# Optimization experiments

Hardware: AMD Instinct MI355X
Metric: run time of the kernel (lower is better)

Reference implementation:

```python
import jax, jax.numpy as jnp
import numpy as np

B = 2048            # number of session graphs in the batch
ORDER = 3           # multi-order granularities s1, s2, s3
D = 128             # input_dim = hidden_dim = output_dim (fc_out is None)
NODES_PER = (50, 25, 16)   # nodes per graph for s1, s2, s3
NPG = sum(NODES_PER)       # 91 nodes per graph (summed batch_num_nodes)
N = B * NPG                # total flattened nodes


def setup_inputs() -> dict:
    key = jax.random.key(0)
    k0, k1, k2, k3 = jax.random.split(key, 4)
    feats = jax.random.normal(k0, (N, D), dtype=jnp.float32)
    scale = 1.0 / np.sqrt(D).astype(np.float32)
    Wu = jax.random.normal(k1, (ORDER, D, D), dtype=jnp.float32) * scale
    bu = jnp.zeros((ORDER, D), dtype=jnp.float32)
    Wv = jax.random.normal(k2, (ORDER, D, D), dtype=jnp.float32) * scale
    We = jax.random.normal(k3, (ORDER, D), dtype=jnp.float32) * scale
    # segment id per node: idx = cat([ones(batch_num_nodes[j]) * j])
    idx = jnp.repeat(jnp.arange(B, dtype=jnp.int32), NPG)
    # last node of each order's block inside every graph (feats['s_i'][last_nodess[i]])
    offs = np.cumsum([0] + list(NODES_PER))
    last = np.stack([np.arange(B) * NPG + (offs[o + 1] - 1) for o in range(ORDER)])
    last_idx = jnp.asarray(last, dtype=jnp.int32)  # [ORDER, B]
    return {"feats": feats, "Wu": Wu, "bu": bu, "Wv": Wv, "We": We,
            "idx": idx, "last_idx": last_idx}


def reference(feats, Wu, bu, Wv, We, idx, last_idx):
    # feat_u = fc_u[i](feats)                        -> [O, N, D]
    feat_u = jnp.einsum('nd,odh->onh', feats, Wu) + bu[:, None, :]
    # feat_v = fc_v[i](feat_vs[:, i])[idx]           -> [O, N, D]
    fv = jnp.einsum('obd,odh->obh', feats[last_idx], Wv)   # [O, B, D]
    feat_v = fv[:, idx, :]                                  # gather per segment id
    # e = fc_e[i](sigmoid(feat_u + feat_v))          -> [N, O]
    e = jnp.einsum('onh,oh->no', jax.nn.sigmoid(feat_u + feat_v), We)
    # alpha = segment_softmax(batch_num_nodes, e), numerically stable
    m = jax.lax.stop_gradient(jax.ops.segment_max(e, idx, num_segments=B))
    ex = jnp.exp(e - m[idx])
    denom = jax.ops.segment_sum(ex, idx, num_segments=B)
    alpha = ex / denom[idx]                                 # [N, O]
    # rst = segment_reduce(batch_num_nodes, feats * alpha, 'sum') -> [B, O, D]
    weighted = alpha[:, :, None] * feats[:, None, :]        # [N, O, D]
    rst = jax.ops.segment_sum(weighted, idx, num_segments=B)
    return rst  # [B, ORDER, D]; fc_out is None and activation is None
```

## Files before the change

### kernel.cpp

```cpp
#include <hip/hip_runtime.h>
#include <hip/hip_bf16.h>
#include <stdint.h>

#define NB 2048
#define D 128
#define NPG 91

typedef __attribute__((ext_vector_type(8))) short short8;
typedef __attribute__((ext_vector_type(4))) float f32x4;

__device__ __forceinline__ unsigned bf16pk(float a, float b) {
  __hip_bfloat162 h2 = __float22bfloat162_rn(make_float2(a, b));
  return *reinterpret_cast<unsigned*>(&h2);
}

__device__ __forceinline__ float sigf(float x) {
  float e = __expf(-x);
  return __builtin_amdgcn_rcpf(1.0f + e);
}

__global__ void w_pack(const float* __restrict__ Wu,
                       const float* __restrict__ Wv,
                       uint4* __restrict__ wpk) {
  const int u = blockIdx.x;
  const float* W = (u < 12) ? Wu : Wv;
  const int uu = (u < 12) ? u : u - 12;
  const int o = uu >> 2, kk = uu & 3;
  const int t = threadIdx.x;
  #pragma unroll
  for (int i = 0; i < 2; ++i) {
    int idx = i * 256 + t;
    int row = idx >> 2, g = idx & 3;
    const float* src = W + (size_t)o * D * D + (kk * 32 + g * 8) * D + row;
    uint4 pk;
    pk.x = bf16pk(src[0 * D], src[1 * D]);
    pk.y = bf16pk(src[2 * D], src[3 * D]);
    pk.z = bf16pk(src[4 * D], src[5 * D]);
    pk.w = bf16pk(src[6 * D], src[7 * D]);
    wpk[(size_t)u * 512 + idx] = pk;
  }
}

__global__ __launch_bounds__(512, 8) void sihg_main(
    const float* __restrict__ feats,
    const uint4* __restrict__ wpk,
    const float* __restrict__ bu,
    const float* __restrict__ We,
    float* __restrict__ out) {
  __shared__ __align__(16) char lds[38016];
  constexpr int FE_OFF  = 0;
  constexpr int BUL_OFF = 24576;
  constexpr int WEL_OFF = 26112;
  constexpr int EP_OFF  = 27648;
  constexpr int AL_OFF  = 36864;

  const int t = threadIdx.x;
  const int b = blockIdx.x;
  const int q = t >> 6;
  const int l = t & 63;
  const int g = l >> 4;
  const int lm = l & 15;

  float* bul = (float*)(lds + BUL_OFF);
  float* wel = (float*)(lds + WEL_OFF);
  float (*ep)[3][96] = (float (*)[3][96])(lds + EP_OFF);
  float (*alpha)[96] = (float (*)[96])(lds + AL_OFF);

  const float* fbase = feats + (size_t)b * NPG * D;

  #pragma unroll 1
  for (int i = 0; i < 3; ++i) {
    int c = t + i * 512;
    int r = c >> 4, d0 = (c & 15) * 8;
    uint4 pk4;
    if (r < NPG) {
      const float* src = fbase + r * D + d0;
      float4 f0 = *(const float4*)(src);
      float4 f1 = *(const float4*)(src + 4);
      pk4.x = bf16pk(f0.x, f0.y);
      pk4.y = bf16pk(f0.z, f0.w);
      pk4.z = bf16pk(f1.x, f1.y);
      pk4.w = bf16pk(f1.z, f1.w);
    } else {
      pk4.x = 0u; pk4.y = 0u; pk4.z = 0u; pk4.w = 0u;
    }
    int off = r * 256 + ((d0 * 2) ^ ((r & 7) << 4));
    *(uint4*)(lds + FE_OFF + off) = pk4;
  }
  if (t < 384) {
    bul[t] = bu[t];
    wel[t] = We[t];
  }
  __syncthreads();

  const int swz = (lm & 7) << 4;
  #pragma unroll 1
  for (int o = 0; o < 3; ++o) {
    const int frow = (o == 0) ? 49 : (o == 1) ? 74 : 90;
    const int fswz = (frow & 7) << 4;
    f32x4 z = {0.f, 0.f, 0.f, 0.f};
    #pragma unroll
    for (int kk = 0; kk < 4; ++kk) {
      short8 av = *(const short8*)&wpk[(size_t)(12 + o * 4 + kk) * 512 + (q * 16 + lm) * 4 + g];
      short8 bv = *(const short8*)(lds + FE_OFF + frow * 256 + ((kk * 64 + g * 16) ^ fswz));
      z = __builtin_amdgcn_mfma_f32_16x16x32_bf16(av, bv, z, 0, 0, 0);
    }
    f32x4 bu4 = *(const f32x4*)&bul[o * 128 + q * 16 + g * 4];
    float bias[4];
    bias[0] = z[0] + bu4[0]; bias[1] = z[1] + bu4[1];
    bias[2] = z[2] + bu4[2]; bias[3] = z[3] + bu4[3];
    f32x4 ww = *(const f32x4*)&wel[o * 128 + q * 16 + g * 4];

    short8 a[4];
    #pragma unroll
    for (int kk = 0; kk < 4; ++kk)
      a[kk] = *(const short8*)&wpk[(size_t)(o * 4 + kk) * 512 + (q * 16 + lm) * 4 + g];

    #pragma unroll 1
    for (int nh = 0; nh < 2; ++nh) {
      f32x4 acc[3];
      #pragma unroll
      for (int j = 0; j < 3; ++j) acc[j] = (f32x4){0.f, 0.f, 0.f, 0.f};

      __builtin_amdgcn_s_setprio(1);
      #pragma unroll
      for (int kk = 0; kk < 4; ++kk) {
        const int cb = kk * 64 + g * 16;
        #pragma unroll
        for (int j = 0; j < 3; ++j) {
          const int nt = nh * 3 + j;
          short8 bv = *(const short8*)(lds + FE_OFF + (nt * 16 + lm) * 256 + (cb ^ swz));
          acc[j] = __builtin_amdgcn_mfma_f32_16x16x32_bf16(a[kk], bv, acc[j], 0, 0, 0);
        }
      }
      __builtin_amdgcn_s_setprio(0);
      #pragma unroll
      for (int j = 0; j < 3; ++j) {
        float e = sigf(acc[j][0] + bias[0]) * ww[0]
                + sigf(acc[j][1] + bias[1]) * ww[1]
                + sigf(acc[j][2] + bias[2]) * ww[2]
                + sigf(acc[j][3] + bias[3]) * ww[3];
        e += __shfl_xor(e, 16);
        e += __shfl_xor(e, 32);
        if (l < 16) ep[q][o][(nh * 3 + j) * 16 + l] = e;
      }
    }
  }

  const int hw = t >> 5;
  const int d4 = (t & 31) * 4;
  float4 pf[6];
  #pragma unroll
  for (int i = 0; i < 6; ++i) {
    int n = hw + 16 * i;
    if (n < NPG) pf[i] = *(const float4*)(fbase + n * D + d4);
  }
  __syncthreads();

  if (q < 3) {
    const int o = q;
    const int n1 = l, n2 = l + 64;
    float x1 = 0.f, x2 = 0.f;
    if (n1 < NPG) {
      float e1 = 0.f;
      #pragma unroll
      for (int j = 0; j < 8; ++j) e1 += ep[j][o][n1];
      x1 = __expf(e1);
    }
    if (n2 < NPG) {
      float e2 = 0.f;
      #pragma unroll
      for (int j = 0; j < 8; ++j) e2 += ep[j][o][n2];
      x2 = __expf(e2);
    }
    float s = x1 + x2;
    #pragma unroll
    for (int m = 1; m < 64; m <<= 1) s += __shfl_xor(s, m);
    float inv = __builtin_amdgcn_rcpf(s);
    if (n1 < NPG) alpha[o][n1] = x1 * inv;
    if (n2 < NPG) alpha[o][n2] = x2 * inv;
  }
  __syncthreads();

  {
    float a0x = 0.f, a0y = 0.f, a0z = 0.f, a0w = 0.f;
    float a1x = 0.f, a1y = 0.f, a1z = 0.f, a1w = 0.f;
    float a2x = 0.f, a2y = 0.f, a2z = 0.f, a2w = 0.f;
    #pragma unroll
    for (int i = 0; i < 6; ++i) {
      int n = hw + 16 * i;
      if (n < NPG) {
        float al0 = alpha[0][n], al1 = alpha[1][n], al2 = alpha[2][n];
        a0x += pf[i].x * al0; a0y += pf[i].y * al0; a0z += pf[i].z * al0; a0w += pf[i].w * al0;
        a1x += pf[i].x * al1; a1y += pf[i].y * al1; a1z += pf[i].z * al1; a1w += pf[i].w * al1;
        a2x += pf[i].x * al2; a2y += pf[i].y * al2; a2z += pf[i].z * al2; a2w += pf[i].w * al2;
      }
    }
    a0x += __shfl_xor(a0x, 32); a0y += __shfl_xor(a0y, 32);
    a0z += __shfl_xor(a0z, 32); a0w += __shfl_xor(a0w, 32);
    a1x += __shfl_xor(a1x, 32); a1y += __shfl_xor(a1y, 32);
    a1z += __shfl_xor(a1z, 32); a1w += __shfl_xor(a1w, 32);
    a2x += __shfl_xor(a2x, 32); a2y += __shfl_xor(a2y, 32);
    a2z += __shfl_xor(a2z, 32); a2w += __shfl_xor(a2w, 32);
    float* part = (float*)(lds + FE_OFF);
    if (l < 32) {
      float4 s0 = {a0x, a0y, a0z, a0w};
      float4 s1 = {a1x, a1y, a1z, a1w};
      float4 s2 = {a2x, a2y, a2z, a2w};
      *(float4*)&part[q * 384 + 0 * 128 + d4] = s0;
      *(float4*)&part[q * 384 + 1 * 128 + d4] = s1;
      *(float4*)&part[q * 384 + 2 * 128 + d4] = s2;
    }
  }
  __syncthreads();
  if (t < 384) {
    const float* part = (const float*)(lds + FE_OFF);
    float s = 0.f;
    #pragma unroll
    for (int j = 0; j < 8; ++j) s += part[j * 384 + t];
    out[(size_t)b * 384 + t] = s;
  }
}

extern "C" void kernel_launch(void* const* d_in, const int* in_sizes, int n_in,
                              void* d_out, int out_size, void* d_ws, size_t ws_size,
                              hipStream_t stream) {
  const float* feats = (const float*)d_in[0];
  const float* Wu    = (const float*)d_in[1];
  const float* bu    = (const float*)d_in[2];
  const float* Wv    = (const float*)d_in[3];
  const float* We    = (const float*)d_in[4];
  float* out = (float*)d_out;
  uint4* wpk = (uint4*)d_ws;

  w_pack<<<24, 256, 0, stream>>>(Wu, Wv, wpk);
  sihg_main<<<NB, 512, 0, stream>>>(feats, wpk, bu, We, out);
}
```

Before: 60.23 us.

## Compute feat_v from global before LDS staging; reuse bf16 LDS feats for pooling

The per-order fc_v projection of the last node is now computed straight from global memory before the LDS fill, and its biased result is stored to LDS once instead of being recomputed by every wave inside the order loop. The final weighted pooling stage stops re-reading fp32 feats from global memory and instead reads the bf16 copy already staged in LDS, widening it back to fp32. This removes a second global pass over the graph's features and some redundant MFMA work per wave. The pooling now uses bf16-rounded features, which lowers accuracy of the output sum.

```diff
diff --git a/kernel.cpp b/kernel.cpp
--- a/kernel.cpp
+++ b/kernel.cpp
@@ -49,7 +49,7 @@
     float* __restrict__ out) {
   __shared__ __align__(16) char lds[38016];
   constexpr int FE_OFF  = 0;
-  constexpr int BUL_OFF = 24576;
+  constexpr int BFV_OFF = 24576;
   constexpr int WEL_OFF = 26112;
   constexpr int EP_OFF  = 27648;
   constexpr int AL_OFF  = 36864;
@@ -61,12 +61,35 @@
   const int g = l >> 4;
   const int lm = l & 15;
 
-  float* bul = (float*)(lds + BUL_OFF);
+  float* bfvp = (float*)(lds + BFV_OFF);
   float* wel = (float*)(lds + WEL_OFF);
   float (*ep)[3][96] = (float (*)[3][96])(lds + EP_OFF);
   float (*alpha)[96] = (float (*)[96])(lds + AL_OFF);
 
   const float* fbase = feats + (size_t)b * NPG * D;
+
+  {
+    #pragma unroll
+    for (int o = 0; o < 3; ++o) {
+      const int frow = (o == 0) ? 49 : (o == 1) ? 74 : 90;
+      const float* frp = fbase + frow * D + g * 8;
+      f32x4 z = {0.f, 0.f, 0.f, 0.f};
+      #pragma unroll
+      for (int kk = 0; kk < 4; ++kk) {
+        short8 av = *(const short8*)&wpk[(size_t)(12 + o * 4 + kk) * 512 + (q * 16 + lm) * 4 + g];
+        float4 f0 = *(const float4*)(frp + kk * 32);
+        float4 f1 = *(const float4*)(frp + kk * 32 + 4);
+        uint4 u = {bf16pk(f0.x, f0.y), bf16pk(f0.z, f0.w),
+                   bf16pk(f1.x, f1.y), bf16pk(f1.z, f1.w)};
+        z = __builtin_amdgcn_mfma_f32_16x16x32_bf16(av, *reinterpret_cast<short8*>(&u), z, 0, 0, 0);
+      }
+      float4 bu4 = *(const float4*)&bu[o * 128 + q * 16 + g * 4];
+      if (lm == 0) {
+        float4 s = {z[0] + bu4.x, z[1] + bu4.y, z[2] + bu4.z, z[3] + bu4.w};
+        *(float4*)&bfvp[o * 128 + q * 16 + g * 4] = s;
+      }
+    }
+  }
 
   #pragma unroll 1
   for (int i = 0; i < 3; ++i) {
@@ -87,29 +110,14 @@
     int off = r * 256 + ((d0 * 2) ^ ((r & 7) << 4));
     *(uint4*)(lds + FE_OFF + off) = pk4;
   }
-  if (t < 384) {
-    bul[t] = bu[t];
-    wel[t] = We[t];
-  }
+  if (t < 384) wel[t] = We[t];
   __syncthreads();
 
   const int swz = (lm & 7) << 4;
   #pragma unroll 1
   for (int o = 0; o < 3; ++o) {
-    const int frow = (o == 0) ? 49 : (o == 1) ? 74 : 90;
-    const int fswz = (frow & 7) << 4;
-    f32x4 z = {0.f, 0.f, 0.f, 0.f};
-    #pragma unroll
-    for (int kk = 0; kk < 4; ++kk) {
-      short8 av = *(const short8*)&wpk[(size_t)(12 + o * 4 + kk) * 512 + (q * 16 + lm) * 4 + g];
-      short8 bv = *(const short8*)(lds + FE_OFF + frow * 256 + ((kk * 64 + g * 16) ^ fswz));
-      z = __builtin_amdgcn_mfma_f32_16x16x32_bf16(av, bv, z, 0, 0, 0);
-    }
-    f32x4 bu4 = *(const f32x4*)&bul[o * 128 + q * 16 + g * 4];
-    float bias[4];
-    bias[0] = z[0] + bu4[0]; bias[1] = z[1] + bu4[1];
-    bias[2] = z[2] + bu4[2]; bias[3] = z[3] + bu4[3];
-    f32x4 ww = *(const f32x4*)&wel[o * 128 + q * 16 + g * 4];
+    f32x4 bias = *(const f32x4*)&bfvp[o * 128 + q * 16 + g * 4];
+    f32x4 ww   = *(const f32x4*)&wel[o * 128 + q * 16 + g * 4];
 
     short8 a[4];
     #pragma unroll
@@ -149,11 +157,16 @@
 
   const int hw = t >> 5;
   const int d4 = (t & 31) * 4;
-  float4 pf[6];
-  #pragma unroll
-  for (int i = 0; i < 6; ++i) {
-    int n = hw + 16 * i;
-    if (n < NPG) pf[i] = *(const float4*)(fbase + n * D + d4);
+  ushort4 pb[6];
+  {
+    const int inb = ((d4 * 2) & ~15);
+    const int lo8 = ((d4 * 2) & 8);
+    #pragma unroll
+    for (int i = 0; i < 6; ++i) {
+      int n = hw + 16 * i;
+      if (n < NPG)
+        pb[i] = *(const ushort4*)(lds + FE_OFF + n * 256 + (inb ^ ((n & 7) << 4)) + lo8);
+    }
   }
   __syncthreads();
 
@@ -190,10 +203,14 @@
     for (int i = 0; i < 6; ++i) {
       int n = hw + 16 * i;
       if (n < NPG) {
+        float fx = __uint_as_float((unsigned)pb[i].x << 16);
+        float fy = __uint_as_float((unsigned)pb[i].y << 16);
+        float fz = __uint_as_float((unsigned)pb[i].z << 16);
+        float fw = __uint_as_float((unsigned)pb[i].w << 16);
         float al0 = alpha[0][n], al1 = alpha[1][n], al2 = alpha[2][n];
-        a0x += pf[i].x * al0; a0y += pf[i].y * al0; a0z += pf[i].z * al0; a0w += pf[i].w * al0;
-        a1x += pf[i].x * al1; a1y += pf[i].y * al1; a1z += pf[i].z * al1; a1w += pf[i].w * al1;
-        a2x += pf[i].x * al2; a2y += pf[i].y * al2; a2z += pf[i].z * al2; a2w += pf[i].w * al2;
+        a0x += fx * al0; a0y += fy * al0; a0z += fz * al0; a0w += fw * al0;
+        a1x += fx * al1; a1y += fy * al1; a1z += fz * al1; a1w += fw * al1;
+        a2x += fx * al2; a2y += fy * al2; a2z += fz * al2; a2w += fw * al2;
       }
     }
     a0x += __shfl_xor(a0x, 32); a0y += __shfl_xor(a0y, 32);
```

Result: slower. 62.44 us (+3.7%).
